# Performance work log

Measured on AMD Instinct MI355X. Metric: run time of the kernel, lower is better.

Reference implementation:

```python
import jax, jax.numpy as jnp
import numpy as np

B, S, HID = 1, 2048, 2048
H, NOPE, ROPE, VDIM = 16, 128, 64, 128
QR, KVR = 1536, 512
IH, ID = 16, 128
TOPK = 512
THETA = 10000.0
EPS = 1e-6
SCALE = (NOPE + ROPE) ** -0.5
NEG = -1e9


def _cos_sin(s, dim, dtype):
    inv = 1.0 / (THETA ** (np.arange(0, dim, 2, dtype=np.float32) / dim))
    t = np.arange(s, dtype=np.float32)
    f = np.outer(t, inv)
    emb = np.concatenate([f, f], -1)
    return jnp.asarray(np.cos(emb), dtype), jnp.asarray(np.sin(emb), dtype)


def _rope(x, cos, sin):
    # x: [b,s,h,d]; cos/sin: [s,d]; NeoX-style rotate_half
    x1, x2 = jnp.split(x, 2, axis=-1)
    rot = jnp.concatenate([-x2, x1], axis=-1)
    return x * cos[None, :, None, :] + rot * sin[None, :, None, :]


def _rmsnorm(x, w):
    v = jnp.mean(x.astype(jnp.float32) ** 2, -1, keepdims=True)
    return (x.astype(jnp.float32) * jax.lax.rsqrt(v + EPS)).astype(x.dtype) * w


def _layernorm(x, w, b):
    m = jnp.mean(x, -1, keepdims=True)
    v = jnp.var(x, -1, keepdims=True)
    return (x - m) * jax.lax.rsqrt(v + EPS) * w + b


def setup_inputs() -> dict:
    key = jax.random.key(0)
    ks = jax.random.split(key, 12)
    g = lambda k, shp: jax.random.normal(k, shp, jnp.float32) * 0.02
    return {
        'hidden_states': jax.random.normal(ks[0], (B, S, HID), jnp.float32),
        'q_a_w': g(ks[1], (QR, HID)),
        'q_a_ln_w': jnp.ones((QR,), jnp.float32),
        'q_b_w': g(ks[2], (H * (NOPE + ROPE), QR)),
        'kv_a_w': g(ks[3], (KVR + ROPE, HID)),
        'kv_a_ln_w': jnp.ones((KVR,), jnp.float32),
        'kv_b_w': g(ks[4], (H * (NOPE + VDIM), KVR)),
        'o_w': g(ks[5], (HID, H * VDIM)),
        'idx_wq_b_w': g(ks[6], (IH * ID, QR)),
        'idx_wk_w': g(ks[7], (ID, HID)),
        'idx_kn_w': jnp.ones((ID,), jnp.float32),
        'idx_kn_b': jnp.zeros((ID,), jnp.float32),
        'idx_wproj_w': g(ks[8], (IH, HID)),
    }


def reference(hidden_states, q_a_w, q_a_ln_w, q_b_w, kv_a_w, kv_a_ln_w, kv_b_w, o_w,
              idx_wq_b_w, idx_wk_w, idx_kn_w, idx_kn_b, idx_wproj_w):
    b, s, _ = hidden_states.shape
    cos, sin = _cos_sin(s, ROPE, hidden_states.dtype)

    # --- MLA projections ---
    qr = _rmsnorm(hidden_states @ q_a_w.T, q_a_ln_w)                 # [b,s,QR]
    q = (qr @ q_b_w.T).reshape(b, s, H, NOPE + ROPE)
    q_nope, q_pe = q[..., :NOPE], q[..., NOPE:]
    q_pe = _rope(q_pe, cos, sin)
    ckv = hidden_states @ kv_a_w.T                                   # [b,s,KVR+ROPE]
    c_kv, k_pe = ckv[..., :KVR], ckv[..., KVR:]
    k_pe = _rope(k_pe[:, :, None, :], cos, sin)                      # [b,s,1,ROPE]
    kv = (_rmsnorm(c_kv, kv_a_ln_w) @ kv_b_w.T).reshape(b, s, H, NOPE + VDIM)
    k_nope, v = kv[..., :NOPE], kv[..., NOPE:]

    # --- DSA indexer: per-token importance scores ---
    iq = (qr @ idx_wq_b_w.T).reshape(b, s, IH, ID)
    iq = jnp.concatenate([_rope(iq[..., :ROPE], cos, sin), iq[..., ROPE:]], -1)
    ik = _layernorm(hidden_states @ idx_wk_w.T, idx_kn_w, idx_kn_b)  # [b,s,ID]
    ik_pe = _rope(ik[:, :, None, :ROPE], cos, sin)[:, :, 0, :]
    ik = jnp.concatenate([ik_pe, ik[..., ROPE:]], -1)
    iw = (hidden_states @ idx_wproj_w.T) * (IH ** -0.5)              # [b,s,IH]
    idx_scores = jnp.einsum('bqh,bhqk->bqk', iw,
                            jax.nn.relu(jnp.einsum('bqhd,bkd->bhqk', iq, ik)))
    causal = jnp.tril(jnp.ones((s, s), bool))
    idx_scores = jnp.where(causal[None], idx_scores, -jnp.inf)
    _, top_idx = jax.lax.top_k(idx_scores, TOPK)                     # [b,s,TOPK]
    bi = jnp.arange(b)[:, None, None]
    qi = jnp.arange(s)[None, :, None]
    keep = jnp.zeros((b, s, s), bool).at[bi, qi, top_idx].set(True)
    allowed = keep & causal[None]                                    # [b,s,s]

    # --- sparse top-k attention (top-k mask to -inf before softmax) ---
    qh = jnp.concatenate([q_nope, q_pe], -1)                         # [b,s,H,192]
    kh = jnp.concatenate([k_nope, jnp.broadcast_to(k_pe, (b, s, H, ROPE))], -1)
    scores = jnp.einsum('bqhd,bkhd->bhqk', qh, kh) * SCALE
    scores = jnp.where(allowed[:, None], scores, NEG)
    attn = jax.nn.softmax(scores, -1)
    out = jnp.einsum('bhqk,bkhd->bqhd', attn, v).reshape(b, s, H * VDIM)
    return out @ o_w.T
```

## Files before the change

### kernel.cpp

```cpp
#include <hip/hip_runtime.h>
#include <hip/hip_bf16.h>
#include <math.h>

#define SEQ 2048
#define HIDD 2048
#define QRANK 1536
#define KVRANK 512
#define TOPK 512
#define EPSF 1e-6f
#define SCALE_ATTN 0.07216878364870323f
#define NCAT 1680

typedef __attribute__((ext_vector_type(8))) short short8v;
typedef __attribute__((ext_vector_type(4))) short short4v;
typedef __attribute__((ext_vector_type(4))) float f32x4;

__device__ inline unsigned short f2bf(float f) {
    unsigned u = __float_as_uint(f);
    unsigned r = (u + 0x7FFFu + ((u >> 16) & 1u)) >> 16;
    return (unsigned short)r;
}
__device__ inline float bf2f(unsigned short b) {
    return __uint_as_float(((unsigned)b) << 16);
}
__device__ inline void split2(float x, unsigned short& h, unsigned short& l) {
    h = f2bf(x);
    l = f2bf(x - bf2f(h));
}

__device__ inline short4v ds_read_tr16(const void* p) {
#if __has_builtin(__builtin_amdgcn_ds_read_tr16_b64)
    return __builtin_amdgcn_ds_read_tr16_b64((short4v*)p);
#else
    const unsigned short* u = (const unsigned short*)p;
    short4v r;
    r[0] = (short)u[0]; r[1] = (short)u[16]; r[2] = (short)u[32]; r[3] = (short)u[48];
    return r;
#endif
}

__global__ void rope_table_kernel(float* __restrict__ cos_t, float* __restrict__ sin_t) {
    int s = blockIdx.x;
    int i = threadIdx.x;
    double inv = pow(10000.0, -((double)(2 * i)) / 64.0);
    double f = (double)s * inv;
    cos_t[s * 32 + i] = (float)cos(f);
    sin_t[s * 32 + i] = (float)sin(f);
}

__global__ __launch_bounds__(256) void cvt_bf16_4_kernel(
    const float* __restrict__ a, int na4, const float* __restrict__ b, int nb4,
    const float* __restrict__ c, int nc4, const float* __restrict__ d, int nd4,
    unsigned short* __restrict__ oa, unsigned short* __restrict__ ob,
    unsigned short* __restrict__ oc, unsigned short* __restrict__ od)
{
    int total = na4 + nb4 + nc4 + nd4;
    for (int i = blockIdx.x * 256 + threadIdx.x; i < total; i += gridDim.x * 256) {
        const float* src; unsigned short* dst; int j = i;
        if (j < na4) { src = a; dst = oa; }
        else if ((j -= na4) < nb4) { src = b; dst = ob; }
        else if ((j -= nb4) < nc4) { src = c; dst = oc; }
        else { j -= nc4; src = d; dst = od; }
        float4 v = ((const float4*)src)[j];
        ushort4 o;
        o.x = f2bf(v.x); o.y = f2bf(v.y); o.z = f2bf(v.z); o.w = f2bf(v.w);
        ((ushort4*)dst)[j] = o;
    }
}

__global__ __launch_bounds__(256) void cvt_split3_kernel(
    const float* __restrict__ hidden, const float* __restrict__ q_a_w,
    const float* __restrict__ idx_wk_w, const float* __restrict__ idx_wproj_w,
    const float* __restrict__ wq,
    unsigned short* __restrict__ hidh, unsigned short* __restrict__ hidl,
    unsigned short* __restrict__ catwh, unsigned short* __restrict__ catwl,
    unsigned short* __restrict__ wqh, unsigned short* __restrict__ wql)
{
    const int nhid4 = HIDD * HIDD / 4;
    const int ncat4 = NCAT * HIDD / 4;
    const int nwq4  = HIDD * QRANK / 4;
    int total = nhid4 + ncat4 + nwq4;
    for (int i = blockIdx.x * 256 + threadIdx.x; i < total; i += gridDim.x * 256) {
        int j = i;
        const float4* s4;
        unsigned short *dh, *dl;
        float scale = 1.f;
        if (j < nhid4) {
            s4 = (const float4*)hidden + j; dh = hidh; dl = hidl;
        } else if ((j -= nhid4) < ncat4) {
            int row = (j * 4) >> 11;
            dh = catwh; dl = catwl;
            if (row < 1536) s4 = (const float4*)q_a_w + j;
            else if (row < 1664) s4 = (const float4*)idx_wk_w + (j - 1536 * 512);
            else { s4 = (const float4*)idx_wproj_w + (j - 1664 * 512); scale = 0.25f; }
        } else {
            j -= ncat4;
            s4 = (const float4*)wq + j; dh = wqh; dl = wql;
        }
        float4 v = *s4;
        float xs[4] = {v.x * scale, v.y * scale, v.z * scale, v.w * scale};
        ushort4 oh, ol;
        unsigned short h2, l2;
        split2(xs[0], h2, l2); oh.x = h2; ol.x = l2;
        split2(xs[1], h2, l2); oh.y = h2; ol.y = l2;
        split2(xs[2], h2, l2); oh.z = h2; ol.z = l2;
        split2(xs[3], h2, l2); oh.w = h2; ol.w = l2;
        ((ushort4*)dh)[j] = oh;
        ((ushort4*)dl)[j] = ol;
    }
}

__global__ __launch_bounds__(256) void wkt_kernel(const float* __restrict__ kvb,
                                                  unsigned short* __restrict__ wkt) {
    __shared__ float t[128][129];
    int h = blockIdx.x, n0 = blockIdx.y * 128;
    int tid = threadIdx.x;
    for (int it = tid; it < 128 * 32; it += 256) {
        int d = it >> 5, c4 = it & 31;
        float4 v = *(const float4*)(kvb + ((size_t)(h * 256 + d)) * 512 + n0 + c4 * 4);
        t[d][c4 * 4 + 0] = v.x; t[d][c4 * 4 + 1] = v.y;
        t[d][c4 * 4 + 2] = v.z; t[d][c4 * 4 + 3] = v.w;
    }
    __syncthreads();
    for (int it = tid; it < 128 * 32; it += 256) {
        int n = it >> 5, dc = it & 31;
        ushort4 o;
        o.x = f2bf(t[dc * 4 + 0][n]); o.y = f2bf(t[dc * 4 + 1][n]);
        o.z = f2bf(t[dc * 4 + 2][n]); o.w = f2bf(t[dc * 4 + 3][n]);
        *(ushort4*)(wkt + ((size_t)h * 512 + n0 + n) * 128 + dc * 4) = o;
    }
}

__global__ __launch_bounds__(256) void gemm_cat_split_kernel(
    const float* __restrict__ hidden, const float* __restrict__ q_a_w,
    const float* __restrict__ idx_wk_w, const float* __restrict__ idx_wproj_w,
    const unsigned short* __restrict__ hidh, const unsigned short* __restrict__ hidl,
    const unsigned short* __restrict__ catwh, const unsigned short* __restrict__ catwl,
    float* __restrict__ ccat)
{
    __shared__ __align__(16) unsigned short Ah[128 * 32], Al[128 * 32];
    __shared__ __align__(16) unsigned short Bh[128 * 32], Bl[128 * 32];
    int tid = threadIdx.x;
    int l = tid & 63, w = tid >> 6;
    int wr = w >> 1, wc = w & 1;
    int m0 = blockIdx.x * 128, n0 = blockIdx.y * 128;
    const bool pre = (hidh != nullptr);
    f32x4 acc[4][4] = {};
    for (int k0 = 0; k0 < HIDD; k0 += 32) {
        __syncthreads();
#pragma unroll
        for (int i = 0; i < 2; ++i) {
            int idx = tid + i * 256;
            int r = idx >> 2, cc = idx & 3;
            int sw = cc ^ (r & 3);
            int gb = n0 + r; if (gb > NCAT - 1) gb = NCAT - 1;
            if (pre) {
                size_t abase = (size_t)(m0 + r) * HIDD + k0 + cc * 8;
                *(short8v*)&Ah[r * 32 + sw * 8] = *(const short8v*)(hidh + abase);
                *(short8v*)&Al[r * 32 + sw * 8] = *(const short8v*)(hidl + abase);
                size_t bbase = (size_t)gb * HIDD + k0 + cc * 8;
                *(short8v*)&Bh[r * 32 + sw * 8] = *(const short8v*)(catwh + bbase);
                *(short8v*)&Bl[r * 32 + sw * 8] = *(const short8v*)(catwl + bbase);
            } else {
                {
                    const float* src = hidden + (size_t)(m0 + r) * HIDD + k0 + cc * 8;
                    float4 f0 = *(const float4*)src, f1 = *(const float4*)(src + 4);
                    float xs[8] = {f0.x, f0.y, f0.z, f0.w, f1.x, f1.y, f1.z, f1.w};
                    short8v dh, dl;
#pragma unroll
                    for (int e = 0; e < 8; ++e) {
                        unsigned short hh, ll; split2(xs[e], hh, ll);
                        dh[e] = (short)hh; dl[e] = (short)ll;
                    }
                    *(short8v*)&Ah[r * 32 + sw * 8] = dh;
                    *(short8v*)&Al[r * 32 + sw * 8] = dl;
                }
                {
                    float scale = 1.f;
                    const float* src;
                    if (gb < 1536) src = q_a_w + (size_t)gb * HIDD;
                    else if (gb < 1664) src = idx_wk_w + (size_t)(gb - 1536) * HIDD;
                    else { src = idx_wproj_w + (size_t)(gb - 1664) * HIDD; scale = 0.25f; }
                    src += k0 + cc * 8;
                    float4 f0 = *(const float4*)src, f1 = *(const float4*)(src + 4);
                    float xs[8] = {f0.x, f0.y, f0.z, f0.w, f1.x, f1.y, f1.z, f1.w};
                    short8v dh, dl;
#pragma unroll
                    for (int e = 0; e < 8; ++e) {
                        unsigned short hh, ll; split2(xs[e] * scale, hh, ll);
                        dh[e] = (short)hh; dl[e] = (short)ll;
                    }
                    *(short8v*)&Bh[r * 32 + sw * 8] = dh;
                    *(short8v*)&Bl[r * 32 + sw * 8] = dl;
                }
            }
        }
        __syncthreads();
        short8v avh[4], avl[4];
#pragma unroll
        for (int mt = 0; mt < 4; ++mt) {
            int row = wr * 64 + mt * 16 + (l & 15);
            int ch = (l >> 4) ^ (row & 3);
            avh[mt] = *(const short8v*)&Ah[row * 32 + ch * 8];
            avl[mt] = *(const short8v*)&Al[row * 32 + ch * 8];
        }
#pragma unroll
        for (int nt = 0; nt < 4; ++nt) {
            int row = wc * 64 + nt * 16 + (l & 15);
            int ch = (l >> 4) ^ (row & 3);
            short8v bvh = *(const short8v*)&Bh[row * 32 + ch * 8];
            short8v bvl = *(const short8v*)&Bl[row * 32 + ch * 8];
#pragma unroll
            for (int mt = 0; mt < 4; ++mt) {
                acc[mt][nt] = __builtin_amdgcn_mfma_f32_16x16x32_bf16(avh[mt], bvh, acc[mt][nt], 0, 0, 0);
                acc[mt][nt] = __builtin_amdgcn_mfma_f32_16x16x32_bf16(avh[mt], bvl, acc[mt][nt], 0, 0, 0);
                acc[mt][nt] = __builtin_amdgcn_mfma_f32_16x16x32_bf16(avl[mt], bvh, acc[mt][nt], 0, 0, 0);
            }
        }
    }
#pragma unroll
    for (int mt = 0; mt < 4; ++mt)
#pragma unroll
        for (int nt = 0; nt < 4; ++nt)
#pragma unroll
            for (int i = 0; i < 4; ++i) {
                int gm = m0 + wr * 64 + mt * 16 + (l >> 4) * 4 + i;
                int gn = n0 + wc * 64 + nt * 16 + (l & 15);
                if (gn < NCAT) ccat[(size_t)gm * NCAT + gn] = acc[mt][nt][i];
            }
}

__global__ __launch_bounds__(256) void gemm_iq_split_kernel(
    const float* __restrict__ qr, const float* __restrict__ wq,
    const unsigned short* __restrict__ qrh, const unsigned short* __restrict__ qrl,
    const unsigned short* __restrict__ wqh, const unsigned short* __restrict__ wql,
    const float* __restrict__ cos_t, const float* __restrict__ sin_t,
    unsigned short* __restrict__ iqh, unsigned short* __restrict__ iql)
{
    __shared__ __align__(16) unsigned short Ah[128 * 32], Al[128 * 32];
    __shared__ __align__(16) unsigned short Bh[128 * 32], Bl[128 * 32];
    int tid = threadIdx.x;
    int l = tid & 63, w = tid >> 6;
    int wr = w >> 1, wc = w & 1;
    int m0 = blockIdx.x * 128, n0 = blockIdx.y * 128;
    int hh_ = blockIdx.y;
    const bool pre = (wqh != nullptr);
    f32x4 acc[4][4] = {};
    for (int k0 = 0; k0 < QRANK; k0 += 32) {
        __syncthreads();
#pragma unroll
        for (int i = 0; i < 2; ++i) {
            int idx = tid + i * 256;
            int r = idx >> 2, cc = idx & 3;
            int sw = cc ^ (r & 3);
            if (pre) {
                size_t abase = (size_t)(m0 + r) * QRANK + k0 + cc * 8;
                *(short8v*)&Ah[r * 32 + sw * 8] = *(const short8v*)(qrh + abase);
                *(short8v*)&Al[r * 32 + sw * 8] = *(const short8v*)(qrl + abase);
                size_t bbase = (size_t)(n0 + r) * QRANK + k0 + cc * 8;
                *(short8v*)&Bh[r * 32 + sw * 8] = *(const short8v*)(wqh + bbase);
                *(short8v*)&Bl[r * 32 + sw * 8] = *(const short8v*)(wql + bbase);
            } else {
                {
                    const float* src = qr + (size_t)(m0 + r) * QRANK + k0 + cc * 8;
                    float4 f0 = *(const float4*)src, f1 = *(const float4*)(src + 4);
                    float xs[8] = {f0.x, f0.y, f0.z, f0.w, f1.x, f1.y, f1.z, f1.w};
                    short8v dh, dl;
#pragma unroll
                    for (int e = 0; e < 8; ++e) {
                        unsigned short h2, l2; split2(xs[e], h2, l2);
                        dh[e] = (short)h2; dl[e] = (short)l2;
                    }
                    *(short8v*)&Ah[r * 32 + sw * 8] = dh;
                    *(short8v*)&Al[r * 32 + sw * 8] = dl;
                }
                {
                    const float* src = wq + (size_t)(n0 + r) * QRANK + k0 + cc * 8;
                    float4 f0 = *(const float4*)src, f1 = *(const float4*)(src + 4);
                    float xs[8] = {f0.x, f0.y, f0.z, f0.w, f1.x, f1.y, f1.z, f1.w};
                    short8v dh, dl;
#pragma unroll
                    for (int e = 0; e < 8; ++e) {
                        unsigned short h2, l2; split2(xs[e], h2, l2);
                        dh[e] = (short)h2; dl[e] = (short)l2;
                    }
                    *(short8v*)&Bh[r * 32 + sw * 8] = dh;
                    *(short8v*)&Bl[r * 32 + sw * 8] = dl;
                }
            }
        }
        __syncthreads();
        short8v avh[4], avl[4];
#pragma unroll
        for (int mt = 0; mt < 4; ++mt) {
            int row = wr * 64 + mt * 16 + (l & 15);
            int ch = (l >> 4) ^ (row & 3);
            avh[mt] = *(const short8v*)&Ah[row * 32 + ch * 8];
            avl[mt] = *(const short8v*)&Al[row * 32 + ch * 8];
        }
#pragma unroll
        for (int nt = 0; nt < 4; ++nt) {
            int row = wc * 64 + nt * 16 + (l & 15);
            int ch = (l >> 4) ^ (row & 3);
            short8v bvh = *(const short8v*)&Bh[row * 32 + ch * 8];
            short8v bvl = *(const short8v*)&Bl[row * 32 + ch * 8];
#pragma unroll
            for (int mt = 0; mt < 4; ++mt) {
                acc[mt][nt] = __builtin_amdgcn_mfma_f32_16x16x32_bf16(avh[mt], bvh, acc[mt][nt], 0, 0, 0);
                acc[mt][nt] = __builtin_amdgcn_mfma_f32_16x16x32_bf16(avh[mt], bvl, acc[mt][nt], 0, 0, 0);
                acc[mt][nt] = __builtin_amdgcn_mfma_f32_16x16x32_bf16(avl[mt], bvh, acc[mt][nt], 0, 0, 0);
            }
        }
    }
    if (wc == 0) {
#pragma unroll
        for (int mt = 0; mt < 4; ++mt)
#pragma unroll
            for (int nt = 0; nt < 2; ++nt)
#pragma unroll
                for (int i = 0; i < 4; ++i) {
                    int q = m0 + wr * 64 + mt * 16 + (l >> 4) * 4 + i;
                    int dd = nt * 16 + (l & 15);
                    float c = cos_t[q * 32 + dd], s = sin_t[q * 32 + dd];
                    float x1 = acc[mt][nt][i], x2 = acc[mt][nt + 2][i];
                    acc[mt][nt][i] = x1 * c - x2 * s;
                    acc[mt][nt + 2][i] = x2 * c + x1 * s;
                }
    }
#pragma unroll
    for (int mt = 0; mt < 4; ++mt)
#pragma unroll
        for (int nt = 0; nt < 4; ++nt)
#pragma unroll
            for (int i = 0; i < 4; ++i) {
                int q = m0 + wr * 64 + mt * 16 + (l >> 4) * 4 + i;
                int d = wc * 64 + nt * 16 + (l & 15);
                size_t idx = ((size_t)q * 16 + hh_) * 128 + d;
                unsigned short h2, l2; split2(acc[mt][nt][i], h2, l2);
                iqh[idx] = h2; iql[idx] = l2;
            }
}

template <typename TA, typename TC>
__global__ __launch_bounds__(256) void mfma_nt_kernel(
    const TA* __restrict__ A, const unsigned short* __restrict__ B, TC* __restrict__ C,
    int M, int N, int K, int lda, int ldb, int ldc, long ab, long bb, long cb,
    const float* __restrict__ cos_t, const float* __restrict__ sin_t, int rope_mode)
{
    __shared__ __align__(16) unsigned short Asl[128 * 32];
    __shared__ __align__(16) unsigned short Bsl[128 * 32];
    int z = blockIdx.z;
    const TA* Az = A + (size_t)z * ab;
    const unsigned short* Bz = B + (size_t)z * bb;
    TC* Cz = C + (size_t)z * cb;
    int tid = threadIdx.x;
    int l = tid & 63, w = tid >> 6;
    int wr = w >> 1, wc = w & 1;
    int m0 = blockIdx.x * 128, n0 = blockIdx.y * 128;
    f32x4 acc[4][4] = {};

    for (int k0 = 0; k0 < K; k0 += 32) {
        __syncthreads();
#pragma unroll
        for (int i = 0; i < 2; ++i) {
            int idx = tid + i * 256;
            int r = idx >> 2, cc = idx & 3;
            int sw = cc ^ (r & 3);
            {
                short8v d;
                const TA* src = Az + (size_t)(m0 + r) * lda + k0 + cc * 8;
                if constexpr (sizeof(TA) == 2) {
                    d = *(const short8v*)src;
                } else {
                    float4 f0 = *(const float4*)src;
                    float4 f1 = *(const float4*)(src + 4);
                    d[0] = (short)f2bf(f0.x); d[1] = (short)f2bf(f0.y);
                    d[2] = (short)f2bf(f0.z); d[3] = (short)f2bf(f0.w);
                    d[4] = (short)f2bf(f1.x); d[5] = (short)f2bf(f1.y);
                    d[6] = (short)f2bf(f1.z); d[7] = (short)f2bf(f1.w);
                }
                *(short8v*)&Asl[r * 32 + sw * 8] = d;
            }
            {
                int gb = n0 + r; if (gb > N - 1) gb = N - 1;
                short8v d = *(const short8v*)(Bz + (size_t)gb * ldb + k0 + cc * 8);
                *(short8v*)&Bsl[r * 32 + sw * 8] = d;
            }
        }
        __syncthreads();
        short8v av[4], bv[4];
#pragma unroll
        for (int mt = 0; mt < 4; ++mt) {
            int row = wr * 64 + mt * 16 + (l & 15);
            int ch = (l >> 4) ^ (row & 3);
            av[mt] = *(const short8v*)&Asl[row * 32 + ch * 8];
        }
#pragma unroll
        for (int nt = 0; nt < 4; ++nt) {
            int row = wc * 64 + nt * 16 + (l & 15);
            int ch = (l >> 4) ^ (row & 3);
            bv[nt] = *(const short8v*)&Bsl[row * 32 + ch * 8];
        }
#pragma unroll
        for (int mt = 0; mt < 4; ++mt)
#pragma unroll
            for (int nt = 0; nt < 4; ++nt)
                acc[mt][nt] = __builtin_amdgcn_mfma_f32_16x16x32_bf16(av[mt], bv[nt], acc[mt][nt], 0, 0, 0);
    }
    if (rope_mode) {
        int gcol64 = (n0 >> 6) + wc;
        bool dorope = (rope_mode == 1) ? ((gcol64 % 3) == 2) : (gcol64 == 8);
        if (dorope) {
#pragma unroll
            for (int mt = 0; mt < 4; ++mt)
#pragma unroll
                for (int nt = 0; nt < 2; ++nt)
#pragma unroll
                    for (int i = 0; i < 4; ++i) {
                        int q = m0 + wr * 64 + mt * 16 + (l >> 4) * 4 + i;
                        int dd = nt * 16 + (l & 15);
                        float c = cos_t[q * 32 + dd], sn = sin_t[q * 32 + dd];
                        float x1 = acc[mt][nt][i], x2 = acc[mt][nt + 2][i];
                        acc[mt][nt][i] = x1 * c - x2 * sn;
                        acc[mt][nt + 2][i] = x2 * c + x1 * sn;
                    }
        }
    }
#pragma unroll
    for (int mt = 0; mt < 4; ++mt) {
#pragma unroll
        for (int nt = 0; nt < 4; ++nt) {
#pragma unroll
            for (int i = 0; i < 4; ++i) {
                int gm = m0 + wr * 64 + mt * 16 + (l >> 4) * 4 + i;
                int gn = n0 + wc * 64 + nt * 16 + (l & 15);
                if (gn < N) {
                    float v = acc[mt][nt][i];
                    if constexpr (sizeof(TC) == 4) Cz[(size_t)gm * ldc + gn] = v;
                    else Cz[(size_t)gm * ldc + gn] = f2bf(v);
                }
            }
        }
    }
}

__global__ __launch_bounds__(256) void rmsnorm_kernel(
    const float* __restrict__ in, const float* __restrict__ w, float* __restrict__ out,
    unsigned short* __restrict__ bf_out, unsigned short* __restrict__ bf_lo,
    int n, int in_stride)
{
    int row = blockIdx.x, tid = threadIdx.x;
    const float* x = in + (size_t)row * in_stride;
    float4 v[2];
    int cnt = 0;
    float ss = 0.f;
    int nf4 = n >> 2;
    for (int i = tid; i < nf4; i += 256) {
        float4 t = *(const float4*)(x + i * 4);
        v[cnt++] = t;
        ss += t.x * t.x + t.y * t.y + t.z * t.z + t.w * t.w;
    }
#pragma unroll
    for (int m = 32; m; m >>= 1) ss += __shfl_xor(ss, m);
    __shared__ float red[8];
    int wid = tid >> 6;
    if ((tid & 63) == 0) red[wid] = ss;
    __syncthreads();
    if (tid == 0) {
        float s = red[0] + red[1] + red[2] + red[3];
        red[4] = rsqrtf(s / (float)n + EPSF);
    }
    __syncthreads();
    float scale = red[4];
    cnt = 0;
    for (int i = tid; i < nf4; i += 256) {
        float4 t = v[cnt++];
        float4 wv = *(const float4*)(w + i * 4);
        float4 o;
        o.x = t.x * scale * wv.x; o.y = t.y * scale * wv.y;
        o.z = t.z * scale * wv.z; o.w = t.w * scale * wv.w;
        *(float4*)(out + (size_t)row * n + i * 4) = o;
        if (bf_out) {
            ushort4 ob;
            ob.x = f2bf(o.x); ob.y = f2bf(o.y); ob.z = f2bf(o.z); ob.w = f2bf(o.w);
            *(ushort4*)(bf_out + (size_t)row * n + i * 4) = ob;
            if (bf_lo) {
                ushort4 ol;
                ol.x = f2bf(o.x - bf2f(ob.x)); ol.y = f2bf(o.y - bf2f(ob.y));
                ol.z = f2bf(o.z - bf2f(ob.z)); ol.w = f2bf(o.w - bf2f(ob.w));
                *(ushort4*)(bf_lo + (size_t)row * n + i * 4) = ol;
            }
        }
    }
}

__global__ __launch_bounds__(256) void rmsnorm_khg_kernel(
    const float* __restrict__ ckv, const float* __restrict__ w,
    unsigned short* __restrict__ khg)
{
    int row = blockIdx.x, tid = threadIdx.x;
    const float* x = ckv + (size_t)row * 576;
    float4 v = make_float4(0.f, 0.f, 0.f, 0.f);
    float ss = 0.f;
    if (tid < 128) {
        v = *(const float4*)(x + tid * 4);
        ss = v.x * v.x + v.y * v.y + v.z * v.z + v.w * v.w;
    }
#pragma unroll
    for (int mm = 32; mm; mm >>= 1) ss += __shfl_xor(ss, mm);
    __shared__ float red[8];
    if ((tid & 63) == 0) red[tid >> 6] = ss;
    __syncthreads();
    if (tid == 0) red[4] = rsqrtf((red[0] + red[1] + red[2] + red[3]) * (1.f / 512.f) + EPSF);
    __syncthreads();
    float scale = red[4];
    if (tid < 128) {
        float4 wv = *(const float4*)(w + tid * 4);
        ushort4 ob;
        ob.x = f2bf(v.x * scale * wv.x); ob.y = f2bf(v.y * scale * wv.y);
        ob.z = f2bf(v.z * scale * wv.z); ob.w = f2bf(v.w * scale * wv.w);
        *(ushort4*)(khg + (size_t)row * 576 + tid * 4) = ob;
    } else if (tid < 192) {
        khg[(size_t)row * 576 + 512 + (tid - 128)] = f2bf(x[512 + tid - 128]);
    }
}

__global__ __launch_bounds__(64) void ln_rope_split_kernel(
    const float* __restrict__ in, int stride,
    const float* __restrict__ w, const float* __restrict__ b,
    const float* __restrict__ cos_t, const float* __restrict__ sin_t,
    unsigned short* __restrict__ ikh, unsigned short* __restrict__ ikl)
{
    int row = blockIdx.x, tid = threadIdx.x;
    const float* x = in + (size_t)row * stride;
    float x0 = x[tid], x1 = x[tid + 64];
    float s = x0 + x1, ss = x0 * x0 + x1 * x1;
#pragma unroll
    for (int m = 32; m; m >>= 1) { s += __shfl_xor(s, m); ss += __shfl_xor(ss, m); }
    float mean = s * (1.f / 128.f);
    float var = ss * (1.f / 128.f) - mean * mean;
    float r = rsqrtf(var + EPSF);
    float n0 = (x0 - mean) * r * w[tid] + b[tid];
    float n1 = (x1 - mean) * r * w[tid + 64] + b[tid + 64];
    float c = cos_t[row * 32 + (tid & 31)], sn = sin_t[row * 32 + (tid & 31)];
    float other = __shfl_xor(n0, 32);
    float r0 = (tid < 32) ? (n0 * c - other * sn) : (n0 * c + other * sn);
    unsigned short h2, l2;
    split2(r0, h2, l2);
    ikh[(size_t)row * 128 + tid] = h2; ikl[(size_t)row * 128 + tid] = l2;
    split2(n1, h2, l2);
    ikh[(size_t)row * 128 + 64 + tid] = h2; ikl[(size_t)row * 128 + 64 + tid] = l2;
}

__global__ __launch_bounds__(256) void idx_scores_mfma_kernel(
    const unsigned short* __restrict__ iqh, const unsigned short* __restrict__ iql,
    const unsigned short* __restrict__ ikh, const unsigned short* __restrict__ ikl,
    const float* __restrict__ iwsrc, int iw_stride,
    float* __restrict__ scores)
{
    int q0 = blockIdx.x * 64, k0 = blockIdx.y * 64;
    int tid = threadIdx.x;
    if (k0 > q0 + 63) {
        for (int t = tid; t < 64 * 64; t += 256) {
            int r = t >> 6, c = t & 63;
            scores[(size_t)(q0 + r) * SEQ + k0 + c] = -INFINITY;
        }
        return;
    }
    __shared__ __align__(16) unsigned short skh[64 * 128], skl[64 * 128];
    __shared__ __align__(16) unsigned short sqh[64 * 128], sql[64 * 128];
    __shared__ float iws[64][16];
    int l = tid & 63, w = tid >> 6;
    for (int it = tid; it < 64 * 16; it += 256) {
        int r = it >> 4, c = it & 15;
        int sw = c ^ (r & 15);
        *(short8v*)&skh[r * 128 + sw * 8] = *(const short8v*)(ikh + (size_t)(k0 + r) * 128 + c * 8);
        *(short8v*)&skl[r * 128 + sw * 8] = *(const short8v*)(ikl + (size_t)(k0 + r) * 128 + c * 8);
    }
    {
        int r = tid >> 2, c = tid & 3;
        *(float4*)&iws[r][c * 4] = *(const float4*)(iwsrc + (size_t)(q0 + r) * iw_stride + c * 4);
    }
    __syncthreads();
    short8v bhr[4][4], blr[4][4];
#pragma unroll
    for (int nt = 0; nt < 4; ++nt)
#pragma unroll
        for (int ks = 0; ks < 4; ++ks) {
            int brow = nt * 16 + (l & 15);
            int bch = ((l >> 4) + ks * 4) ^ (brow & 15);
            bhr[nt][ks] = *(const short8v*)&skh[brow * 128 + bch * 8];
            blr[nt][ks] = *(const short8v*)&skl[brow * 128 + bch * 8];
        }
    f32x4 acc[4] = {};
    for (int h = 0; h < 16; ++h) {
        __syncthreads();
        for (int it = tid; it < 64 * 16; it += 256) {
            int r = it >> 4, c = it & 15;
            int sw = c ^ (r & 15);
            size_t base = ((size_t)(q0 + r) * 16 + h) * 128 + c * 8;
            *(short8v*)&sqh[r * 128 + sw * 8] = *(const short8v*)(iqh + base);
            *(short8v*)&sql[r * 128 + sw * 8] = *(const short8v*)(iql + base);
        }
        __syncthreads();
        f32x4 dot[4] = {};
#pragma unroll
        for (int ks = 0; ks < 4; ++ks) {
            int arow = w * 16 + (l & 15);
            int ach = ((l >> 4) + ks * 4) ^ (arow & 15);
            short8v ah = *(const short8v*)&sqh[arow * 128 + ach * 8];
            short8v al = *(const short8v*)&sql[arow * 128 + ach * 8];
#pragma unroll
            for (int nt = 0; nt < 4; ++nt) {
                dot[nt] = __builtin_amdgcn_mfma_f32_16x16x32_bf16(ah, bhr[nt][ks], dot[nt], 0, 0, 0);
                dot[nt] = __builtin_amdgcn_mfma_f32_16x16x32_bf16(ah, blr[nt][ks], dot[nt], 0, 0, 0);
                dot[nt] = __builtin_amdgcn_mfma_f32_16x16x32_bf16(al, bhr[nt][ks], dot[nt], 0, 0, 0);
            }
        }
#pragma unroll
        for (int nt = 0; nt < 4; ++nt)
#pragma unroll
            for (int i = 0; i < 4; ++i) {
                float wv = iws[w * 16 + (l >> 4) * 4 + i][h];
                acc[nt][i] += wv * fmaxf(dot[nt][i], 0.f);
            }
    }
#pragma unroll
    for (int nt = 0; nt < 4; ++nt)
#pragma unroll
        for (int i = 0; i < 4; ++i) {
            int q = q0 + w * 16 + (l >> 4) * 4 + i;
            int k = k0 + nt * 16 + (l & 15);
            scores[(size_t)q * SEQ + k] = (k <= q) ? acc[nt][i] : -INFINITY;
        }
}

__global__ __launch_bounds__(1024) void topk_kernel(
    const float* __restrict__ scores, int* __restrict__ sel)
{
    int qi = blockIdx.x, tid = threadIdx.x;
    __shared__ unsigned long long keys[2048];
    const float* srow = scores + (size_t)qi * SEQ;
#pragma unroll
    for (int r = 0; r < 2; ++r) {
        int k = tid + r * 1024;
        unsigned u = __float_as_uint(srow[k]);
        unsigned mv = (u & 0x80000000u) ? ~u : (u | 0x80000000u);
        keys[k] = ((unsigned long long)mv << 32) | (unsigned)(2047 - k);
    }
    for (int ksz = 2; ksz <= 2048; ksz <<= 1) {
        for (int j = ksz >> 1; j > 0; j >>= 1) {
            __syncthreads();
#pragma unroll 1
            for (int r = 0; r < 2; ++r) {
                int i = tid + r * 1024;
                int ixj = i ^ j;
                if (ixj > i) {
                    unsigned long long a = keys[i], b = keys[ixj];
                    bool dir = ((i & ksz) == 0);
                    if ((a < b) == dir) { keys[i] = b; keys[ixj] = a; }
                }
            }
        }
    }
    __syncthreads();
    if (tid < TOPK) {
        int k = 2047 - (int)(keys[tid] & 0xFFFFFFFFu);
        sel[(size_t)qi * TOPK + tid] = (tid <= qi) ? k : -1;
    }
}

__global__ __launch_bounds__(256) void attn_mfma_kernel(
    const unsigned short* __restrict__ qabs,
    const float* __restrict__ qsrc,
    const unsigned short* __restrict__ khg,
    const int* __restrict__ sel,
    unsigned short* __restrict__ ocomp)
{
    __shared__ __align__(16) char smem[77312];
    unsigned short* plds = (unsigned short*)(smem + 74752);
    float* smax = (float*)(smem + 76800);
    float* ssum = (float*)(smem + 77056);

    const int qi = blockIdx.x;
    const int tid = threadIdx.x;
    const int l = tid & 63, w = tid >> 6;
    const int lg = l >> 4, lr = l & 15;
    const int nv = min(TOPK, qi + 1);
    const int ntile = (nv + 63) >> 6;
    const int krow = w * 16 + lr;

    const int ck = tid >> 6, cc = tid & 63;
    const int pk = tid >> 3, pc = tid & 7;
    const int* selrow = sel + (size_t)qi * TOPK;

    short8v aq[18];
    {
        const unsigned short* qa = qabs + ((size_t)qi * 16 + lr) * 512 + lg * 8;
#pragma unroll
        for (int ks = 0; ks < 16; ++ks)
            aq[ks] = *(const short8v*)(qa + ks * 32);
        const float* qp = qsrc + (size_t)qi * 3072 + lr * 192 + 128 + lg * 8;
#pragma unroll
        for (int ks = 0; ks < 2; ++ks) {
            float4 f0 = *(const float4*)(qp + ks * 32);
            float4 f1 = *(const float4*)(qp + ks * 32 + 4);
            short8v d;
            d[0] = (short)f2bf(f0.x); d[1] = (short)f2bf(f0.y);
            d[2] = (short)f2bf(f0.z); d[3] = (short)f2bf(f0.w);
            d[4] = (short)f2bf(f1.x); d[5] = (short)f2bf(f1.y);
            d[6] = (short)f2bf(f1.z); d[7] = (short)f2bf(f1.w);
            aq[16 + ks] = d;
        }
    }

    short8v vreg[16], preg[2];
#pragma unroll
    for (int j = 0; j < 16; ++j) {
        int sv = selrow[ck + 4 * j];
        if (sv < 0) sv = 0;
        vreg[j] = *(const short8v*)(khg + (size_t)sv * 576 + cc * 8);
    }
#pragma unroll
    for (int j = 0; j < 2; ++j) {
        int sv = selrow[pk + 32 * j];
        if (sv < 0) sv = 0;
        preg[j] = *(const short8v*)(khg + (size_t)sv * 576 + 512 + pc * 8);
    }

    const int sbase = krow * 32 + (lg >> 1) * 2080 + (lg & 1) * 16;
    const int vboff = w * 16640 + lg * 256 + lr * 2;

    float m[4] = {-1e30f, -1e30f, -1e30f, -1e30f};
    float lsum[4] = {0.f, 0.f, 0.f, 0.f};
    f32x4 oacc[8] = {};

    for (int t = 0; t < ntile; ++t) {
        const int j0 = t * 64;
        __syncthreads();
#pragma unroll
        for (int j = 0; j < 16; ++j) {
            int key = ck + 4 * j;
            *(short8v*)(smem + (cc >> 1) * 2080 + key * 32 + (cc & 1) * 16) = vreg[j];
        }
#pragma unroll
        for (int j = 0; j < 2; ++j) {
            int key = pk + 32 * j;
            *(short8v*)(smem + 66560 + ((key * 128 + pc * 16) ^ ((key & 7) << 4))) = preg[j];
        }
        __syncthreads();
        if (t + 1 < ntile) {
            int j1 = j0 + 64;
#pragma unroll
            for (int j = 0; j < 16; ++j) {
                int sv = selrow[j1 + ck + 4 * j];
                if (sv < 0) sv = 0;
                vreg[j] = *(const short8v*)(khg + (size_t)sv * 576 + cc * 8);
            }
#pragma unroll
            for (int j = 0; j < 2; ++j) {
                int sv = selrow[j1 + pk + 32 * j];
                if (sv < 0) sv = 0;
                preg[j] = *(const short8v*)(khg + (size_t)sv * 576 + 512 + pc * 8);
            }
        }
        f32x4 s = {};
#pragma unroll
        for (int ks = 0; ks < 16; ++ks) {
            short8v b = *(const short8v*)(smem + sbase + ks * 4160);
            s = __builtin_amdgcn_mfma_f32_16x16x32_bf16(aq[ks], b, s, 0, 0, 0);
        }
#pragma unroll
        for (int ks = 0; ks < 2; ++ks) {
            short8v b = *(const short8v*)(smem + 66560 +
                ((krow * 128 + ks * 64 + lg * 16) ^ ((krow & 7) << 4)));
            s = __builtin_amdgcn_mfma_f32_16x16x32_bf16(aq[16 + ks], b, s, 0, 0, 0);
        }
        bool kvalid = (j0 + krow) < nv;
#pragma unroll
        for (int i = 0; i < 4; ++i)
            s[i] = kvalid ? s[i] * SCALE_ATTN : -1e30f;
        float tm[4];
#pragma unroll
        for (int i = 0; i < 4; ++i) tm[i] = s[i];
#pragma unroll
        for (int sh = 1; sh < 16; sh <<= 1)
#pragma unroll
            for (int i = 0; i < 4; ++i) tm[i] = fmaxf(tm[i], __shfl_xor(tm[i], sh));
        if (lr == 0) *(float4*)&smax[w * 16 + lg * 4] = make_float4(tm[0], tm[1], tm[2], tm[3]);
        __syncthreads();
        float mn[4], scl[4];
#pragma unroll
        for (int i = 0; i < 4; ++i) {
            int h = lg * 4 + i;
            float tmax = fmaxf(fmaxf(smax[h], smax[16 + h]), fmaxf(smax[32 + h], smax[48 + h]));
            mn[i] = fmaxf(m[i], tmax);
            scl[i] = __expf(m[i] - mn[i]);
            m[i] = mn[i];
        }
        float p[4], rs[4];
#pragma unroll
        for (int i = 0; i < 4; ++i) { p[i] = __expf(s[i] - mn[i]); rs[i] = p[i]; }
#pragma unroll
        for (int sh = 1; sh < 16; sh <<= 1)
#pragma unroll
            for (int i = 0; i < 4; ++i) rs[i] += __shfl_xor(rs[i], sh);
        if (lr == 0) *(float4*)&ssum[w * 16 + lg * 4] = make_float4(rs[0], rs[1], rs[2], rs[3]);
        {
            ushort4 pb;
            pb.x = f2bf(p[0]); pb.y = f2bf(p[1]); pb.z = f2bf(p[2]); pb.w = f2bf(p[3]);
            *(ushort4*)&plds[(w * 16 + lr) * 16 + lg * 4] = pb;
        }
        __syncthreads();
#pragma unroll
        for (int i = 0; i < 4; ++i) {
            int h = lg * 4 + i;
            float ts = ssum[h] + ssum[16 + h] + ssum[32 + h] + ssum[48 + h];
            lsum[i] = lsum[i] * scl[i] + ts;
        }
#pragma unroll
        for (int nt = 0; nt < 8; ++nt)
#pragma unroll
            for (int i = 0; i < 4; ++i) oacc[nt][i] *= scl[i];
#pragma unroll
        for (int kb = 0; kb < 2; ++kb) {
            short8v af;
#pragma unroll
            for (int j = 0; j < 8; ++j)
                af[j] = (short)plds[(kb * 32 + lg * 8 + j) * 16 + lr];
#pragma unroll
            for (int nt = 0; nt < 8; ++nt) {
                const char* a = smem + vboff + kb * 1024 + nt * 2080;
                short4v t0 = ds_read_tr16(a);
                short4v t1 = ds_read_tr16(a + 128);
                short8v bf = __builtin_shufflevector(t0, t1, 0, 1, 2, 3, 4, 5, 6, 7);
                oacc[nt] = __builtin_amdgcn_mfma_f32_16x16x32_bf16(af, bf, oacc[nt], 0, 0, 0);
            }
        }
    }
    float inv[4];
#pragma unroll
    for (int i = 0; i < 4; ++i) inv[i] = 1.f / lsum[i];
    unsigned short* ob = ocomp + (size_t)qi * 16 * 512;
#pragma unroll
    for (int nt = 0; nt < 8; ++nt) {
        int d = w * 128 + nt * 16 + lr;
#pragma unroll
        for (int i = 0; i < 4; ++i) {
            int h = lg * 4 + i;
            ob[h * 512 + d] = f2bf(oacc[nt][i] * inv[i]);
        }
    }
}

extern "C" void kernel_launch(void* const* d_in, const int* in_sizes, int n_in,
                              void* d_out, int out_size, void* d_ws, size_t ws_size,
                              hipStream_t stream) {
    (void)in_sizes; (void)n_in; (void)out_size;
    const float* hidden      = (const float*)d_in[0];
    const float* q_a_w       = (const float*)d_in[1];
    const float* q_a_ln_w    = (const float*)d_in[2];
    const float* q_b_w       = (const float*)d_in[3];
    const float* kv_a_w      = (const float*)d_in[4];
    const float* kv_a_ln_w   = (const float*)d_in[5];
    const float* kv_b_w      = (const float*)d_in[6];
    const float* o_w         = (const float*)d_in[7];
    const float* idx_wq_b_w  = (const float*)d_in[8];
    const float* idx_wk_w    = (const float*)d_in[9];
    const float* idx_kn_w    = (const float*)d_in[10];
    const float* idx_kn_b    = (const float*)d_in[11];
    const float* idx_wproj_w = (const float*)d_in[12];
    float* out = (float*)d_out;

    char* ws = (char*)d_ws;
    size_t off = 0;
    auto alloc = [&](size_t nbytes) -> void* {
        void* p = ws + off;
        off = (off + nbytes + 255) & ~(size_t)255;
        return p;
    };
    float* cos_t = (float*)alloc((size_t)SEQ * 32 * 4);
    float* sin_t = (float*)alloc((size_t)SEQ * 32 * 4);
    float* qbuf  = (float*)alloc((size_t)SEQ * 3072 * 4);
    float* ckv   = (float*)alloc((size_t)SEQ * 576 * 4);
    int*   sel   = (int*)alloc((size_t)SEQ * TOPK * 4);
    unsigned short* khg      = (unsigned short*)alloc((size_t)SEQ * 576 * 2);
    unsigned short* attno_bf = (unsigned short*)alloc((size_t)SEQ * 2048 * 2);
    unsigned short* qr_bf    = (unsigned short*)alloc((size_t)SEQ * QRANK * 2);
    unsigned short* q_b_bf   = (unsigned short*)alloc((size_t)3072 * QRANK * 2);
    unsigned short* kv_a_bf  = (unsigned short*)alloc((size_t)576 * HIDD * 2);
    unsigned short* o_w_bf   = (unsigned short*)alloc((size_t)HIDD * 2048 * 2);
    unsigned short* kv_b_bf  = (unsigned short*)alloc((size_t)4096 * 512 * 2);
    unsigned short* wkt      = (unsigned short*)alloc((size_t)16 * 512 * 128 * 2);
    size_t mark = off;
    float* qr    = (float*)alloc((size_t)SEQ * QRANK * 4);
    float* ccat  = (float*)alloc((size_t)SEQ * NCAT * 4);
    float* scores = (float*)alloc((size_t)SEQ * SEQ * 4);
    unsigned short* iqh = (unsigned short*)alloc((size_t)SEQ * 2048 * 2);
    unsigned short* iql = (unsigned short*)alloc((size_t)SEQ * 2048 * 2);
    unsigned short* ikh = (unsigned short*)alloc((size_t)SEQ * 128 * 2);
    unsigned short* ikl = (unsigned short*)alloc((size_t)SEQ * 128 * 2);
    unsigned short* hidh  = (unsigned short*)alloc((size_t)HIDD * HIDD * 2);
    unsigned short* hidl  = (unsigned short*)alloc((size_t)HIDD * HIDD * 2);
    unsigned short* catwh = (unsigned short*)alloc((size_t)NCAT * HIDD * 2);
    unsigned short* catwl = (unsigned short*)alloc((size_t)NCAT * HIDD * 2);
    unsigned short* wqh   = (unsigned short*)alloc((size_t)HIDD * QRANK * 2);
    unsigned short* wql   = (unsigned short*)alloc((size_t)HIDD * QRANK * 2);
    unsigned short* qr_l  = (unsigned short*)alloc((size_t)SEQ * QRANK * 2);
    bool fast = (off <= ws_size);
    if (!fast) {
        hidh = hidl = catwh = catwl = wqh = wql = qr_l = nullptr;
    }
    off = mark;
    unsigned short* qabsb = (unsigned short*)alloc((size_t)SEQ * 16 * 512 * 2);
    unsigned short* ocomp = (unsigned short*)alloc((size_t)SEQ * 16 * 512 * 2);

    rope_table_kernel<<<dim3(SEQ), dim3(32), 0, stream>>>(cos_t, sin_t);

    cvt_bf16_4_kernel<<<2048, 256, 0, stream>>>(
        q_b_w, 3072 * QRANK / 4, kv_a_w, 576 * HIDD / 4,
        o_w, HIDD * 2048 / 4, kv_b_w, 4096 * 512 / 4,
        q_b_bf, kv_a_bf, o_w_bf, kv_b_bf);
    wkt_kernel<<<dim3(16, 4), 256, 0, stream>>>(kv_b_w, wkt);
    if (fast)
        cvt_split3_kernel<<<2048, 256, 0, stream>>>(
            hidden, q_a_w, idx_wk_w, idx_wproj_w, idx_wq_b_w,
            hidh, hidl, catwh, catwl, wqh, wql);

    gemm_cat_split_kernel<<<dim3(16, 14), 256, 0, stream>>>(
        hidden, q_a_w, idx_wk_w, idx_wproj_w, hidh, hidl, catwh, catwl, ccat);

    rmsnorm_kernel<<<SEQ, 256, 0, stream>>>(ccat, q_a_ln_w, qr, qr_bf, qr_l, QRANK, NCAT);

    ln_rope_split_kernel<<<SEQ, 64, 0, stream>>>(ccat + 1536, NCAT, idx_kn_w, idx_kn_b, cos_t, sin_t, ikh, ikl);

    mfma_nt_kernel<unsigned short, float><<<dim3(16, 24, 1), 256, 0, stream>>>(
        qr_bf, q_b_bf, qbuf, SEQ, 3072, QRANK, QRANK, QRANK, 3072, 0L, 0L, 0L,
        cos_t, sin_t, 1);

    mfma_nt_kernel<float, float><<<dim3(16, 5, 1), 256, 0, stream>>>(
        hidden, kv_a_bf, ckv, SEQ, 576, HIDD, HIDD, HIDD, 576, 0L, 0L, 0L,
        cos_t, sin_t, 2);
    rmsnorm_khg_kernel<<<SEQ, 256, 0, stream>>>(ckv, kv_a_ln_w, khg);

    gemm_iq_split_kernel<<<dim3(16, 16), 256, 0, stream>>>(
        qr, idx_wq_b_w, qr_bf, qr_l, wqh, wql, cos_t, sin_t, iqh, iql);

    idx_scores_mfma_kernel<<<dim3(32, 32), 256, 0, stream>>>(iqh, iql, ikh, ikl, ccat + 1664, NCAT, scores);
    topk_kernel<<<SEQ, 1024, 0, stream>>>(scores, sel);

    mfma_nt_kernel<float, unsigned short><<<dim3(16, 4, 16), 256, 0, stream>>>(
        qbuf, wkt, qabsb, SEQ, 512, 128, 3072, 128, 16 * 512,
        192L, 512L * 128L, 512L, nullptr, nullptr, 0);

    attn_mfma_kernel<<<SEQ, 256, 0, stream>>>(qabsb, qbuf, khg, sel, ocomp);

    mfma_nt_kernel<unsigned short, unsigned short><<<dim3(16, 1, 16), 256, 0, stream>>>(
        ocomp, kv_b_bf + (size_t)128 * 512, attno_bf, SEQ, 128, 512,
        16 * 512, 512, 2048, 512L, 256L * 512L, 128L, nullptr, nullptr, 0);

    mfma_nt_kernel<unsigned short, float><<<dim3(16, 16, 1), 256, 0, stream>>>(
        attno_bf, o_w_bf, out, SEQ, HIDD, 2048, 2048, 2048, HIDD, 0L, 0L, 0L,
        nullptr, nullptr, 0);
}
```

Baseline: 883.9 us.

## Fold rope table into conversion kernel and drop attention register prefetch

```diff
diff --git a/kernel.cpp b/kernel.cpp
--- a/kernel.cpp
+++ b/kernel.cpp
@@ -39,21 +39,20 @@
 #endif
 }
 
-__global__ void rope_table_kernel(float* __restrict__ cos_t, float* __restrict__ sin_t) {
-    int s = blockIdx.x;
-    int i = threadIdx.x;
-    double inv = pow(10000.0, -((double)(2 * i)) / 64.0);
-    double f = (double)s * inv;
-    cos_t[s * 32 + i] = (float)cos(f);
-    sin_t[s * 32 + i] = (float)sin(f);
-}
-
 __global__ __launch_bounds__(256) void cvt_bf16_4_kernel(
     const float* __restrict__ a, int na4, const float* __restrict__ b, int nb4,
     const float* __restrict__ c, int nc4, const float* __restrict__ d, int nd4,
     unsigned short* __restrict__ oa, unsigned short* __restrict__ ob,
-    unsigned short* __restrict__ oc, unsigned short* __restrict__ od)
-{
+    unsigned short* __restrict__ oc, unsigned short* __restrict__ od,
+    float* __restrict__ cos_t, float* __restrict__ sin_t)
+{
+    if (blockIdx.x < SEQ && threadIdx.x < 32) {
+        int s = blockIdx.x, i = threadIdx.x;
+        double inv = pow(10000.0, -((double)(2 * i)) / 64.0);
+        double f = (double)s * inv;
+        cos_t[s * 32 + i] = (float)cos(f);
+        sin_t[s * 32 + i] = (float)sin(f);
+    }
     int total = na4 + nb4 + nc4 + nd4;
     for (int i = blockIdx.x * 256 + threadIdx.x; i < total; i += gridDim.x * 256) {
         const float* src; unsigned short* dst; int j = i;
@@ -714,20 +713,6 @@
         }
     }
 
-    short8v vreg[16], preg[2];
-#pragma unroll
-    for (int j = 0; j < 16; ++j) {
-        int sv = selrow[ck + 4 * j];
-        if (sv < 0) sv = 0;
-        vreg[j] = *(const short8v*)(khg + (size_t)sv * 576 + cc * 8);
-    }
-#pragma unroll
-    for (int j = 0; j < 2; ++j) {
-        int sv = selrow[pk + 32 * j];
-        if (sv < 0) sv = 0;
-        preg[j] = *(const short8v*)(khg + (size_t)sv * 576 + 512 + pc * 8);
-    }
-
     const int sbase = krow * 32 + (lg >> 1) * 2080 + (lg & 1) * 16;
     const int vboff = w * 16640 + lg * 256 + lr * 2;
 
@@ -740,30 +725,20 @@
         __syncthreads();
 #pragma unroll
         for (int j = 0; j < 16; ++j) {
-            int key = ck + 4 * j;
-            *(short8v*)(smem + (cc >> 1) * 2080 + key * 32 + (cc & 1) * 16) = vreg[j];
+            int sv = selrow[j0 + ck + 4 * j];
+            if (sv < 0) sv = 0;
+            short8v v = *(const short8v*)(khg + (size_t)sv * 576 + cc * 8);
+            *(short8v*)(smem + (cc >> 1) * 2080 + (ck + 4 * j) * 32 + (cc & 1) * 16) = v;
         }
 #pragma unroll
         for (int j = 0; j < 2; ++j) {
+            int sv = selrow[j0 + pk + 32 * j];
+            if (sv < 0) sv = 0;
+            short8v v = *(const short8v*)(khg + (size_t)sv * 576 + 512 + pc * 8);
             int key = pk + 32 * j;
-            *(short8v*)(smem + 66560 + ((key * 128 + pc * 16) ^ ((key & 7) << 4))) = preg[j];
-        }
-        __syncthreads();
-        if (t + 1 < ntile) {
-            int j1 = j0 + 64;
-#pragma unroll
-            for (int j = 0; j < 16; ++j) {
-                int sv = selrow[j1 + ck + 4 * j];
-                if (sv < 0) sv = 0;
-                vreg[j] = *(const short8v*)(khg + (size_t)sv * 576 + cc * 8);
-            }
-#pragma unroll
-            for (int j = 0; j < 2; ++j) {
-                int sv = selrow[j1 + pk + 32 * j];
-                if (sv < 0) sv = 0;
-                preg[j] = *(const short8v*)(khg + (size_t)sv * 576 + 512 + pc * 8);
-            }
-        }
+            *(short8v*)(smem + 66560 + ((key * 128 + pc * 16) ^ ((key & 7) << 4))) = v;
+        }
+        __syncthreads();
         f32x4 s = {};
 #pragma unroll
         for (int ks = 0; ks < 16; ++ks) {
@@ -915,12 +890,10 @@
     unsigned short* qabsb = (unsigned short*)alloc((size_t)SEQ * 16 * 512 * 2);
     unsigned short* ocomp = (unsigned short*)alloc((size_t)SEQ * 16 * 512 * 2);
 
-    rope_table_kernel<<<dim3(SEQ), dim3(32), 0, stream>>>(cos_t, sin_t);
-
     cvt_bf16_4_kernel<<<2048, 256, 0, stream>>>(
         q_b_w, 3072 * QRANK / 4, kv_a_w, 576 * HIDD / 4,
         o_w, HIDD * 2048 / 4, kv_b_w, 4096 * 512 / 4,
-        q_b_bf, kv_a_bf, o_w_bf, kv_b_bf);
+        q_b_bf, kv_a_bf, o_w_bf, kv_b_bf, cos_t, sin_t);
     wkt_kernel<<<dim3(16, 4), 256, 0, stream>>>(kv_b_w, wkt);
     if (fast)
         cvt_split3_kernel<<<2048, 256, 0, stream>>>(
```

Measured after the change: 802.8 us, median of 2. -9.2%, faster.
